# Performance work log

Hardware: AMD Instinct MI355X
Metric: run time of the kernel (lower is better)

## Reference

```python
import jax, jax.numpy as jnp
import numpy as np

# Irreps structure (hardcoded per init_kwargs):
#  input  = 16x0e + 8x1o  -> dim 16 + 8*3 = 40
#  query  = key = 8x0e + 4x1o -> dim 8 + 4*3 = 20
#  output = 16x0e + 8x1o -> dim 40
#  edge_sh = 1x0e + 1x1o -> dim 4
M0, M1 = 16, 8          # input multiplicities (scalar, vector)
Q0, Q1 = 8, 4           # query/key multiplicities
O0, O1 = 16, 8          # output multiplicities
TPK_NUMEL = M0*Q0 + M1*Q0 + M0*Q1 + M1*Q1 + M1*Q1   # 320
TPV_NUMEL = M0*O0 + M1*O0 + M0*O1 + M1*O1 + M1*O1   # 640
EDGE_BASIS = 16
HIDDEN = 32


def _split(x):
    """Split irreps vector [*, m0 + 3*m1] into scalars [*, m0] and vectors [*, m1, 3]."""
    m0 = x.shape[-1] - 3 * ((x.shape[-1] - M0) // 3) if False else None
    return x  # placeholder, not used


def fc_net(x, w1, w2):
    """e3nn FullyConnectedNet: no biases, 1/sqrt(fan_in) scaling, silu hidden act."""
    h = jax.nn.silu((x @ w1) * (1.0 / np.sqrt(x.shape[-1])))
    return (h @ w2) * (1.0 / np.sqrt(w1.shape[-1]))


def fctp_edge(xs, xv, shs, shv, w, o0, o1):
    """FullyConnectedTensorProduct((m0x0e+m1x1o) x (1x0e+1x1o) -> (o0x0e+o1x1o))
    with per-edge weights w [E, numel]. Component-normalized CG, path-normalized output.
    xs:[E,m0] xv:[E,m1,3] shs:[E,1] shv:[E,3]."""
    m0, m1 = xs.shape[1], xv.shape[1]
    sizes = [m0*o0, m1*o0, m0*o1, m1*o1, m1*o1]
    offs = np.cumsum([0] + sizes)
    w1 = w[:, offs[0]:offs[1]].reshape(-1, m0, o0)
    w2 = w[:, offs[1]:offs[2]].reshape(-1, m1, o0)
    w3 = w[:, offs[2]:offs[3]].reshape(-1, m0, o1)
    w4 = w[:, offs[3]:offs[4]].reshape(-1, m1, o1)
    w5 = w[:, offs[4]:offs[5]].reshape(-1, m1, o1)
    # scalar output paths: 0e x 0e -> 0e ; 1o x 1o -> 0e (dot / sqrt3)
    p_ss = xs * shs                                            # [E,m0]
    p_vv = jnp.einsum('eic,ec->ei', xv, shv) * (1.0/np.sqrt(3.0))  # [E,m1]
    out_s = (jnp.einsum('ei,eio->eo', p_ss, w1)
             + jnp.einsum('ei,eio->eo', p_vv, w2)) * (1.0/np.sqrt(m0 + m1))
    # vector output paths: 0e x 1o ; 1o x 0e ; 1o x 1o -> 1o (cross / sqrt2)
    p_sv = xs[:, :, None] * shv[:, None, :]                    # [E,m0,3]
    p_vs = xv * shs[:, :, None]                                # [E,m1,3]
    p_xx = jnp.cross(xv, shv[:, None, :]) * (1.0/np.sqrt(2.0)) # [E,m1,3]
    out_v = (jnp.einsum('eic,eio->eoc', p_sv, w3)
             + jnp.einsum('eic,eio->eoc', p_vs, w4)
             + jnp.einsum('eic,eio->eoc', p_xx, w5)) * (1.0/np.sqrt(m0 + 2*m1))
    return out_s, out_v


def setup_inputs() -> dict:
    key = jax.random.key(0)
    ks = jax.random.split(key, 12)
    N, E = 10000, 100000
    node_ft = jax.random.normal(ks[0], (N, M0 + 3*M1), dtype=jnp.float32)
    edge_index = jax.random.randint(ks[1], (2, E), 0, N, dtype=jnp.int64)
    edge_sh = jax.random.normal(ks[2], (E, 4), dtype=jnp.float32)
    edge_scalars = jax.random.uniform(ks[3], (E, EDGE_BASIS), dtype=jnp.float32)
    # learned parameters
    w_q_s = jax.random.normal(ks[4], (M0, Q0), dtype=jnp.float32)
    w_q_v = jax.random.normal(ks[5], (M1, Q1), dtype=jnp.float32)
    fck_w1 = jax.random.normal(ks[6], (EDGE_BASIS, HIDDEN), dtype=jnp.float32)
    fck_w2 = jax.random.normal(ks[7], (HIDDEN, TPK_NUMEL), dtype=jnp.float32)
    fcv_w1 = jax.random.normal(ks[8], (EDGE_BASIS, HIDDEN), dtype=jnp.float32)
    fcv_w2 = jax.random.normal(ks[9], (HIDDEN, TPV_NUMEL), dtype=jnp.float32)
    wdot_s = jax.random.normal(ks[10], (Q0, Q0), dtype=jnp.float32)
    wdot_v = jax.random.normal(ks[11], (Q1, Q1), dtype=jnp.float32)
    return dict(node_ft=node_ft, edge_index=edge_index, edge_sh=edge_sh,
                edge_scalars=edge_scalars, w_q_s=w_q_s, w_q_v=w_q_v,
                fck_w1=fck_w1, fck_w2=fck_w2, fcv_w1=fcv_w1, fcv_w2=fcv_w2,
                wdot_s=wdot_s, wdot_v=wdot_v)


def reference(node_ft, edge_index, edge_sh, edge_scalars, w_q_s, w_q_v,
              fck_w1, fck_w2, fcv_w1, fcv_w2, wdot_s, wdot_v):
    N = node_ft.shape[0]
    sender, receiver = edge_index[0], edge_index[1]
    x_s = node_ft[:, :M0]                       # [N,16]
    x_v = node_ft[:, M0:].reshape(N, M1, 3)     # [N,8,3]
    # q = o3.Linear(input -> query): per-irrep linear mixing, 1/sqrt(mul) norm
    q_s = (x_s @ w_q_s) * (1.0/np.sqrt(M0))                    # [N,Q0]
    q_v = jnp.einsum('nic,io->noc', x_v, w_q_v) * (1.0/np.sqrt(M1))  # [N,Q1,3]
    sh_s, sh_v = edge_sh[:, :1], edge_sh[:, 1:4]
    xs_e, xv_e = x_s[sender], x_v[sender]       # gather sender features
    # per-edge tensor-product weights from radial MLPs
    wk = fc_net(edge_scalars, fck_w1, fck_w2)   # [E, 320]
    wv = fc_net(edge_scalars, fcv_w1, fcv_w2)   # [E, 640]
    k_s, k_v = fctp_edge(xs_e, xv_e, sh_s, sh_v, wk, Q0, Q1)
    v_s, v_v = fctp_edge(xs_e, xv_e, sh_s, sh_v, wv, O0, O1)
    # dot = FCTP(query, key -> 0e) with shared internal weights
    qr_s, qr_v = q_s[receiver], q_v[receiver]
    fan = Q0*Q0 + Q1*Q1
    dot = (jnp.einsum('ei,ej,ij->e', qr_s, k_s, wdot_s)
           + jnp.einsum('eic,ejc,ij->e', qr_v, k_v, wdot_v) * (1.0/np.sqrt(3.0))
           ) * (1.0/np.sqrt(fan))               # [E]
    # scatter-softmax over receiver
    ex = jnp.exp(dot)
    z = jax.ops.segment_sum(ex, receiver, num_segments=N)      # [N]
    alpha = ex / z[receiver]
    a = jnp.sqrt(jax.nn.relu(alpha))            # [E]
    out_s = jax.ops.segment_sum(a[:, None] * v_s, receiver, num_segments=N)
    out_v = jax.ops.segment_sum(a[:, None, None] * v_v, receiver, num_segments=N)
    return jnp.concatenate([out_s, out_v.reshape(N, O1*3)], axis=-1)  # [N,40]
```

## Files before the change

kernel.cpp:

```cpp
#include <hip/hip_runtime.h>


#define BS 256
#define EPB 64

typedef _Float16 h2 __attribute__((ext_vector_type(2)));

__device__ __forceinline__ float silu_f(float x) {
    return x * (1.0f / (1.0f + __expf(-x)));
}
__device__ __forceinline__ unsigned short f2h(float f) {
    return __builtin_bit_cast(unsigned short, (_Float16)f);
}
__device__ __forceinline__ unsigned pk2h(float a, float b) {
    return (unsigned)f2h(a) | ((unsigned)f2h(b) << 16);
}
__device__ __forceinline__ h2 uh2(unsigned u) {
    return __builtin_bit_cast(h2, u);
}
__device__ __forceinline__ h2 pkrtz(float a, float b) {
    return __builtin_bit_cast(h2, __builtin_amdgcn_cvt_pkrtz(a, b));
}
__device__ __forceinline__ h2 pfma(h2 a, h2 b, h2 c) {
    return __builtin_elementwise_fma(a, b, c);
}
__device__ __forceinline__ float h2s(h2 a) {
    return (float)a[0] + (float)a[1];
}
__device__ __forceinline__ float wred4(float v) {
    v += __shfl_xor(v, 16);
    v += __shfl_xor(v, 32);
    return v;
}

__global__ __launch_bounds__(256) void pre_count(
    const float* __restrict__ node_ft,
    const int*   __restrict__ ei,
    const float* __restrict__ w_q_s, const float* __restrict__ w_q_v,
    const float* __restrict__ wdot_s, const float* __restrict__ wdot_v,
    const float* __restrict__ fck_w2, const float* __restrict__ fcv_w2,
    float* __restrict__ qd, int* __restrict__ cnt, int* __restrict__ flag,
    uint4* __restrict__ pk,
    int N, int E)
{
    const int gid = blockIdx.x * blockDim.x + threadIdx.x;

    int acc = 0;
    if ((threadIdx.x & 63) == 0) {
        const int kmax = (E < 64) ? E : 64;
        for (int k = 0; k < kmax; ++k) acc |= ei[2*k + 1];
    }
    acc = __shfl(acc, 0, 64);
    const int is64 = (acc == 0) ? 1 : 0;
    if (gid == 0) *flag = is64;

    if (gid < E) {
        const int rcv = is64 ? ei[2*(E + gid)] : ei[E + gid];
        atomicAdd(cnt + rcv, 1);
    }

    if (gid < 3840) {
        uint4 r;
        if (gid < 1280) {
            const int pg = gid / 320;
            const int local = gid - pg * 320;
            if (local < 128) {
                const int j = local >> 2, rr = local & 3, ip = rr >> 1, h = rr & 1;
                const int i0 = 4*pg + 2*ip;
                const float* s0 = fck_w2 + j*320 + i0*8 + 4*h;
                const float* s1 = s0 + 8;
                r = make_uint4(pk2h(s0[0], s1[0]), pk2h(s0[1], s1[1]),
                               pk2h(s0[2], s1[2]), pk2h(s0[3], s1[3]));
            } else if (local < 192) {
                const int l = local - 128; const int j = l >> 1, ip = l & 1;
                const int i0 = 4*pg + 2*ip;
                const float* s0 = fck_w2 + j*320 + 192 + i0*4;
                const float* s1 = s0 + 4;
                r = make_uint4(pk2h(s0[0], s1[0]), pk2h(s0[1], s1[1]),
                               pk2h(s0[2], s1[2]), pk2h(s0[3], s1[3]));
            } else if (local < 256) {
                const int l = local - 192; const int j = l >> 1, h = l & 1;
                const int i0 = 2*pg;
                const float* s0 = fck_w2 + j*320 + 128 + i0*8 + 4*h;
                const float* s1 = s0 + 8;
                r = make_uint4(pk2h(s0[0], s1[0]), pk2h(s0[1], s1[1]),
                               pk2h(s0[2], s1[2]), pk2h(s0[3], s1[3]));
            } else {
                const int l = local - 256; const int jp = l >> 2, rr = l & 3;
                const int il = rr >> 1, h = rr & 1;
                const int i = 2*pg + il, j0 = 2*jp;
                const int col = (h == 0 ? 256 : 288) + i*4;
                const float* s0 = fck_w2 + j0*320 + col;
                const float* s1 = s0 + 320;
                r = make_uint4(pk2h(s0[0], s1[0]), pk2h(s0[1], s1[1]),
                               pk2h(s0[2], s1[2]), pk2h(s0[3], s1[3]));
            }
        } else if (gid < 2816) {
            const int l2 = gid - 1280;
            const int pg = l2 / 384;
            const int local = l2 - pg * 384;
            const float* s0;
            const float* s1;
            if (local < 256) {
                const int j = local >> 3, rr = local & 7, ip = rr >> 2, h = rr & 3;
                const int i0 = 4*pg + 2*ip;
                s0 = fcv_w2 + j*640 + i0*16 + h*4;
                s1 = s0 + 16;
            } else {
                const int l = local - 256; const int j = l >> 2, h = l & 3;
                const int i0 = 2*pg;
                s0 = fcv_w2 + j*640 + 256 + i0*16 + h*4;
                s1 = s0 + 16;
            }
            r = make_uint4(pk2h(s0[0], s1[0]), pk2h(s0[1], s1[1]),
                           pk2h(s0[2], s1[2]), pk2h(s0[3], s1[3]));
        } else {
            const int l2 = gid - 2816;
            const int pg = l2 >> 8;
            const int local = l2 & 255;
            const float* s0;
            const float* s1;
            if (local < 128) {
                const int j = local >> 2, rr = local & 3, ip = rr >> 1, h = rr & 1;
                const int i0 = 4*pg + 2*ip;
                s0 = fcv_w2 + j*640 + 384 + i0*8 + 4*h;
                s1 = s0 + 8;
            } else {
                const int l = local - 128;
                const int jp = l >> 3, rr = l & 7, il = rr >> 2, h2c = rr & 3;
                const int i = 2*pg + il, j0 = 2*jp;
                const int base = (h2c < 2) ? 512 : 576;
                s0 = fcv_w2 + j0*640 + base + i*8 + (h2c & 1)*4;
                s1 = s0 + 640;
            }
            r = make_uint4(pk2h(s0[0], s1[0]), pk2h(s0[1], s1[1]),
                           pk2h(s0[2], s1[2]), pk2h(s0[3], s1[3]));
        }
        pk[gid] = r;
    }

    const int n = gid;
    if (n >= N) return;

    const float* nf = node_ft + (size_t)n * 40;
    float xs[16];
#pragma unroll
    for (int i = 0; i < 16; ++i) xs[i] = nf[i];
    float qv0[8];
#pragma unroll
    for (int o = 0; o < 8; ++o) {
        float a = 0.f;
#pragma unroll
        for (int i = 0; i < 16; ++i) a += xs[i] * w_q_s[i*8 + o];
        qv0[o] = a * 0.25f;
    }
    float* qdn = qd + (size_t)n * 20;
#pragma unroll
    for (int j = 0; j < 8; ++j) {
        float a = 0.f;
#pragma unroll
        for (int i = 0; i < 8; ++i) a += qv0[i] * wdot_s[i*8 + j];
        qdn[j] = a;
    }
    float xv[8][3];
#pragma unroll
    for (int i = 0; i < 8; ++i)
#pragma unroll
        for (int c = 0; c < 3; ++c) xv[i][c] = nf[16 + i*3 + c];
    float qv[4][3];
#pragma unroll
    for (int o = 0; o < 4; ++o)
#pragma unroll
        for (int c = 0; c < 3; ++c) {
            float a = 0.f;
#pragma unroll
            for (int i = 0; i < 8; ++i) a += xv[i][c] * w_q_v[i*4 + o];
            qv[o][c] = a * 0.35355339059327379f;
        }
#pragma unroll
    for (int j = 0; j < 4; ++j)
#pragma unroll
        for (int c = 0; c < 3; ++c) {
            float a = 0.f;
#pragma unroll
            for (int i = 0; i < 4; ++i) a += qv[i][c] * wdot_v[i*4 + j];
            qdn[8 + j*3 + c] = a;
        }
}

__global__ __launch_bounds__(1024) void scan_kernel(
    const int* __restrict__ cnt, int* __restrict__ start,
    int* __restrict__ cursor, int N)
{
    __shared__ int wsum[16];
    __shared__ int s_carry;
    const int tid = threadIdx.x, wave = tid >> 6, lane = tid & 63;
    if (tid == 0) s_carry = 0;
    __syncthreads();
    for (int base = 0; base < N; base += 1024) {
        const int i = base + tid;
        const int v = (i < N) ? cnt[i] : 0;
        int x = v;
#pragma unroll
        for (int d = 1; d < 64; d <<= 1) {
            const int y = __shfl_up(x, d, 64);
            if (lane >= d) x += y;
        }
        if (lane == 63) wsum[wave] = x;
        __syncthreads();
        if (wave == 0 && lane < 16) {
            int w = wsum[lane];
#pragma unroll
            for (int d = 1; d < 16; d <<= 1) {
                const int y = __shfl_up(w, d, 64);
                if (lane >= d) w += y;
            }
            wsum[lane] = w;
        }
        __syncthreads();
        const int woff = (wave == 0) ? 0 : wsum[wave - 1];
        const int carry = s_carry;
        if (i < N) {
            const int s = carry + woff + x - v;
            start[i] = s;
            cursor[i] = s;
        }
        __syncthreads();
        if (tid == 0) s_carry = carry + wsum[15];
        __syncthreads();
    }
    if (tid == 0) start[N] = s_carry;
}

__global__ __launch_bounds__(BS) void edge_all(
    const float* __restrict__ node_ft,
    const int*   __restrict__ ei,
    const float* __restrict__ edge_sh,
    const float* __restrict__ edge_scalars,
    const float* __restrict__ fck_w1,
    const float* __restrict__ fcv_w1,
    const uint4* __restrict__ pk,
    const float* __restrict__ qd,
    int*   __restrict__ cursor,
    float* __restrict__ vbuf,
    const int* __restrict__ flag,
    int N, int E)
{
    __shared__ uint4 swz[4 * 385];

    const int tid = threadIdx.x;
    const int lane = tid & 63;
    const int p = lane >> 4;
    const int q = lane & 15;
    const int w = tid >> 6;
    const int e = blockIdx.x * EPB + w * 16 + q;
    const bool val = (e < E);
    const int ec = val ? e : (E - 1);

    const int is64 = *flag;
    const int snd = is64 ? ei[2*ec]       : ei[ec];
    const int rcv = is64 ? ei[2*(E + ec)] : ei[E + ec];

    int pos = 0;
    if (p == 0 && val) pos = atomicAdd(cursor + rcv, 1);

    const float4 s4 = *(const float4*)(edge_sh + (size_t)ec * 4);
    const float sh_s = s4.x;
    const float sh_v[3] = {s4.y, s4.z, s4.w};
    const float* nf = node_ft + (size_t)snd * 40;
    const float c3 = 0.57735026918962576f;
    const float c7 = 0.70710678118654752f;

    float es[16];
    {
        const float4* a0 = (const float4*)(edge_scalars + (size_t)ec * 16);
#pragma unroll
        for (int t = 0; t < 4; ++t) {
            const float4 v = a0[t];
            es[4*t+0]=v.x; es[4*t+1]=v.y; es[4*t+2]=v.z; es[4*t+3]=v.w;
        }
    }

#pragma unroll
    for (int it = 0; it < 5; ++it) {
        const int idx = it * BS + tid;
        const int pg = idx / 320;
        swz[pg * 321 + (idx - pg * 320)] = pk[idx];
    }

    float sa = 0.f;
    float hk[32];
#pragma unroll
    for (int j = 0; j < 32; ++j) {
        float a = 0.f;
#pragma unroll
        for (int t = 0; t < 16; ++t) a += es[t] * fck_w1[t*32 + j];
        hk[j] = silu_f(a * 0.25f);
    }
    __syncthreads();

    {
        const uint4* g = swz + p * 321;

        const h2 xs01 = pkrtz(nf[4*p + 0], nf[4*p + 1]);
        const h2 xs23 = pkrtz(nf[4*p + 2], nf[4*p + 3]);
        const float x00 = nf[16 + 6*p], x01 = nf[17 + 6*p], x02 = nf[18 + 6*p];
        const float x10 = nf[19 + 6*p], x11 = nf[20 + 6*p], x12 = nf[21 + 6*p];
        const h2 pvp = pkrtz((x00*sh_v[0] + x01*sh_v[1] + x02*sh_v[2]) * c3,
                             (x10*sh_v[0] + x11*sh_v[1] + x12*sh_v[2]) * c3);

        h2 K1[8] = {}, K3[4] = {}, K2[8] = {};
#pragma unroll
        for (int j = 0; j < 32; ++j) {
            const uint4 A = g[j*4+0], B = g[j*4+1], C = g[j*4+2], D = g[j*4+3];
            const uint4 Ea = g[128 + j*2], Fb = g[128 + j*2 + 1];
            const uint4 U = g[192 + j*2], V = g[192 + j*2 + 1];
            const h2 hh = pkrtz(hk[j], hk[j]);
            const h2 t01 = hh * xs01, t23 = hh * xs23, tp = hh * pvp;
            K1[0]=pfma(t01,uh2(A.x),K1[0]); K1[0]=pfma(t23,uh2(C.x),K1[0]);
            K1[1]=pfma(t01,uh2(A.y),K1[1]); K1[1]=pfma(t23,uh2(C.y),K1[1]);
            K1[2]=pfma(t01,uh2(A.z),K1[2]); K1[2]=pfma(t23,uh2(C.z),K1[2]);
            K1[3]=pfma(t01,uh2(A.w),K1[3]); K1[3]=pfma(t23,uh2(C.w),K1[3]);
            K1[4]=pfma(t01,uh2(B.x),K1[4]); K1[4]=pfma(t23,uh2(D.x),K1[4]);
            K1[5]=pfma(t01,uh2(B.y),K1[5]); K1[5]=pfma(t23,uh2(D.y),K1[5]);
            K1[6]=pfma(t01,uh2(B.z),K1[6]); K1[6]=pfma(t23,uh2(D.z),K1[6]);
            K1[7]=pfma(t01,uh2(B.w),K1[7]); K1[7]=pfma(t23,uh2(D.w),K1[7]);
            K3[0]=pfma(t01,uh2(Ea.x),K3[0]); K3[0]=pfma(t23,uh2(Fb.x),K3[0]);
            K3[1]=pfma(t01,uh2(Ea.y),K3[1]); K3[1]=pfma(t23,uh2(Fb.y),K3[1]);
            K3[2]=pfma(t01,uh2(Ea.z),K3[2]); K3[2]=pfma(t23,uh2(Fb.z),K3[2]);
            K3[3]=pfma(t01,uh2(Ea.w),K3[3]); K3[3]=pfma(t23,uh2(Fb.w),K3[3]);
            K2[0]=pfma(tp,uh2(U.x),K2[0]); K2[1]=pfma(tp,uh2(U.y),K2[1]);
            K2[2]=pfma(tp,uh2(U.z),K2[2]); K2[3]=pfma(tp,uh2(U.w),K2[3]);
            K2[4]=pfma(tp,uh2(V.x),K2[4]); K2[5]=pfma(tp,uh2(V.y),K2[5]);
            K2[6]=pfma(tp,uh2(V.z),K2[6]); K2[7]=pfma(tp,uh2(V.w),K2[7]);
        }

        h2 P4[8] = {}, P5[8] = {};
#pragma unroll
        for (int jp = 0; jp < 16; ++jp) {
            const uint4 a4 = g[256 + jp*4 + 0];
            const uint4 b4 = g[256 + jp*4 + 1];
            const uint4 c4 = g[256 + jp*4 + 2];
            const uint4 d4 = g[256 + jp*4 + 3];
            const h2 hp = pkrtz(hk[2*jp], hk[2*jp+1]);
            P4[0]=pfma(hp,uh2(a4.x),P4[0]); P4[1]=pfma(hp,uh2(a4.y),P4[1]);
            P4[2]=pfma(hp,uh2(a4.z),P4[2]); P4[3]=pfma(hp,uh2(a4.w),P4[3]);
            P5[0]=pfma(hp,uh2(b4.x),P5[0]); P5[1]=pfma(hp,uh2(b4.y),P5[1]);
            P5[2]=pfma(hp,uh2(b4.z),P5[2]); P5[3]=pfma(hp,uh2(b4.w),P5[3]);
            P4[4]=pfma(hp,uh2(c4.x),P4[4]); P4[5]=pfma(hp,uh2(c4.y),P4[5]);
            P4[6]=pfma(hp,uh2(c4.z),P4[6]); P4[7]=pfma(hp,uh2(c4.w),P4[7]);
            P5[4]=pfma(hp,uh2(d4.x),P5[4]); P5[5]=pfma(hp,uh2(d4.y),P5[5]);
            P5[6]=pfma(hp,uh2(d4.z),P5[6]); P5[7]=pfma(hp,uh2(d4.w),P5[7]);
        }

        float ds = 0.f, dv = 0.f;
        {
            float qdr[20];
            const float4* rp = (const float4*)(qd + (size_t)rcv * 20);
#pragma unroll
            for (int t = 0; t < 5; ++t) {
                const float4 a = rp[t];
                qdr[4*t+0]=a.x; qdr[4*t+1]=a.y; qdr[4*t+2]=a.z; qdr[4*t+3]=a.w;
            }
#pragma unroll
            for (int o = 0; o < 8; ++o)
                ds += qdr[o] * (sh_s*h2s(K1[o]) + h2s(K2[o]));
            float KV[12] = {};
            {
                const float s0=sh_s*x00, s1=sh_s*x01, s2=sh_s*x02;
                const float cx0=c7*(x01*sh_v[2]-x02*sh_v[1]);
                const float cx1=c7*(x02*sh_v[0]-x00*sh_v[2]);
                const float cx2=c7*(x00*sh_v[1]-x01*sh_v[0]);
#pragma unroll
                for (int o = 0; o < 4; ++o) {
                    const float w4 = h2s(P4[o]), w5 = h2s(P5[o]);
                    KV[o*3+0] += s0*w4 + cx0*w5;
                    KV[o*3+1] += s1*w4 + cx1*w5;
                    KV[o*3+2] += s2*w4 + cx2*w5;
                }
            }
            {
                const float s0=sh_s*x10, s1=sh_s*x11, s2=sh_s*x12;
                const float cx0=c7*(x11*sh_v[2]-x12*sh_v[1]);
                const float cx1=c7*(x12*sh_v[0]-x10*sh_v[2]);
                const float cx2=c7*(x10*sh_v[1]-x11*sh_v[0]);
#pragma unroll
                for (int o = 0; o < 4; ++o) {
                    const float w4 = h2s(P4[4+o]), w5 = h2s(P5[4+o]);
                    KV[o*3+0] += s0*w4 + cx0*w5;
                    KV[o*3+1] += s1*w4 + cx1*w5;
                    KV[o*3+2] += s2*w4 + cx2*w5;
                }
            }
#pragma unroll
            for (int o = 0; o < 4; ++o) {
                const float k3 = h2s(K3[o]);
#pragma unroll
                for (int c = 0; c < 3; ++c)
                    dv += qdr[8 + o*3 + c] * (k3*sh_v[c] + KV[o*3+c]);
            }
        }
        ds = wred4(ds); dv = wred4(dv);

        if (p == 0 && val) {
            const float dot = ds * 4.0343567508008e-3f + dv * 2.0171788261497e-3f;
            sa = __expf(0.5f * dot);
            vbuf[(size_t)pos * 44 + 40] = sa * sa;
        }
    }

    __syncthreads();
#pragma unroll
    for (int it = 0; it < 6; ++it) {
        const int idx = it * BS + tid;
        const int pg = idx / 384;
        swz[pg * 385 + (idx - pg * 384)] = pk[1280 + idx];
    }

    float hv[32];
#pragma unroll
    for (int j = 0; j < 32; ++j) {
        float a = 0.f;
#pragma unroll
        for (int t = 0; t < 16; ++t) a += es[t] * fcv_w1[t*32 + j];
        hv[j] = silu_f(a * 0.25f);
    }
    __syncthreads();

    {
        const uint4* g = swz + p * 385;

        const h2 xs01 = pkrtz(nf[4*p + 0]*sh_s, nf[4*p + 1]*sh_s);
        const h2 xs23 = pkrtz(nf[4*p + 2]*sh_s, nf[4*p + 3]*sh_s);
        const h2 pvp = pkrtz(
            (nf[16+6*p]*sh_v[0] + nf[17+6*p]*sh_v[1] + nf[18+6*p]*sh_v[2]) * c3,
            (nf[19+6*p]*sh_v[0] + nf[20+6*p]*sh_v[1] + nf[21+6*p]*sh_v[2]) * c3);

        h2 Aa[16] = {};
#pragma unroll
        for (int j = 0; j < 32; ++j) {
            const uint4* gw = g + j*8;
            const uint4 a0 = gw[0], a1 = gw[1], a2 = gw[2], a3 = gw[3];
            const uint4 b0 = gw[4], b1 = gw[5], b2 = gw[6], b3 = gw[7];
            const uint4* g2 = g + 256 + j*4;
            const uint4 u0 = g2[0], u1 = g2[1], u2 = g2[2], u3 = g2[3];
            const h2 hh = pkrtz(hv[j], hv[j]);
            const h2 t01 = hh * xs01, t23 = hh * xs23, tp = hh * pvp;
            Aa[0] =pfma(t01,uh2(a0.x),Aa[0]);  Aa[0] =pfma(t23,uh2(b0.x),Aa[0]);  Aa[0] =pfma(tp,uh2(u0.x),Aa[0]);
            Aa[1] =pfma(t01,uh2(a0.y),Aa[1]);  Aa[1] =pfma(t23,uh2(b0.y),Aa[1]);  Aa[1] =pfma(tp,uh2(u0.y),Aa[1]);
            Aa[2] =pfma(t01,uh2(a0.z),Aa[2]);  Aa[2] =pfma(t23,uh2(b0.z),Aa[2]);  Aa[2] =pfma(tp,uh2(u0.z),Aa[2]);
            Aa[3] =pfma(t01,uh2(a0.w),Aa[3]);  Aa[3] =pfma(t23,uh2(b0.w),Aa[3]);  Aa[3] =pfma(tp,uh2(u0.w),Aa[3]);
            Aa[4] =pfma(t01,uh2(a1.x),Aa[4]);  Aa[4] =pfma(t23,uh2(b1.x),Aa[4]);  Aa[4] =pfma(tp,uh2(u1.x),Aa[4]);
            Aa[5] =pfma(t01,uh2(a1.y),Aa[5]);  Aa[5] =pfma(t23,uh2(b1.y),Aa[5]);  Aa[5] =pfma(tp,uh2(u1.y),Aa[5]);
            Aa[6] =pfma(t01,uh2(a1.z),Aa[6]);  Aa[6] =pfma(t23,uh2(b1.z),Aa[6]);  Aa[6] =pfma(tp,uh2(u1.z),Aa[6]);
            Aa[7] =pfma(t01,uh2(a1.w),Aa[7]);  Aa[7] =pfma(t23,uh2(b1.w),Aa[7]);  Aa[7] =pfma(tp,uh2(u1.w),Aa[7]);
            Aa[8] =pfma(t01,uh2(a2.x),Aa[8]);  Aa[8] =pfma(t23,uh2(b2.x),Aa[8]);  Aa[8] =pfma(tp,uh2(u2.x),Aa[8]);
            Aa[9] =pfma(t01,uh2(a2.y),Aa[9]);  Aa[9] =pfma(t23,uh2(b2.y),Aa[9]);  Aa[9] =pfma(tp,uh2(u2.y),Aa[9]);
            Aa[10]=pfma(t01,uh2(a2.z),Aa[10]); Aa[10]=pfma(t23,uh2(b2.z),Aa[10]); Aa[10]=pfma(tp,uh2(u2.z),Aa[10]);
            Aa[11]=pfma(t01,uh2(a2.w),Aa[11]); Aa[11]=pfma(t23,uh2(b2.w),Aa[11]); Aa[11]=pfma(tp,uh2(u2.w),Aa[11]);
            Aa[12]=pfma(t01,uh2(a3.x),Aa[12]); Aa[12]=pfma(t23,uh2(b3.x),Aa[12]); Aa[12]=pfma(tp,uh2(u3.x),Aa[12]);
            Aa[13]=pfma(t01,uh2(a3.y),Aa[13]); Aa[13]=pfma(t23,uh2(b3.y),Aa[13]); Aa[13]=pfma(tp,uh2(u3.y),Aa[13]);
            Aa[14]=pfma(t01,uh2(a3.z),Aa[14]); Aa[14]=pfma(t23,uh2(b3.z),Aa[14]); Aa[14]=pfma(tp,uh2(u3.z),Aa[14]);
            Aa[15]=pfma(t01,uh2(a3.w),Aa[15]); Aa[15]=pfma(t23,uh2(b3.w),Aa[15]); Aa[15]=pfma(tp,uh2(u3.w),Aa[15]);
        }

        float A0[16];
#pragma unroll
        for (int o = 0; o < 16; ++o) A0[o] = wred4(h2s(Aa[o]));

        if (p == 0 && val) {
            const float cs = 0.03608439182435161f;
            float4* vp = (float4*)(vbuf + (size_t)pos * 44);
#pragma unroll
            for (int t = 0; t < 4; ++t) {
                float4 r;
                r.x = sa * A0[4*t+0] * cs; r.y = sa * A0[4*t+1] * cs;
                r.z = sa * A0[4*t+2] * cs; r.w = sa * A0[4*t+3] * cs;
                vp[t] = r;
            }
        }
    }

    __syncthreads();
#pragma unroll
    for (int it = 0; it < 4; ++it) {
        const int idx = it * BS + tid;
        const int pg = idx >> 8;
        swz[pg * 257 + (idx & 255)] = pk[2816 + idx];
    }
    __syncthreads();

    {
        const uint4* g = swz + p * 257;

        const h2 xs01 = pkrtz(nf[4*p + 0], nf[4*p + 1]);
        const h2 xs23 = pkrtz(nf[4*p + 2], nf[4*p + 3]);

        h2 T3[8] = {};
#pragma unroll
        for (int j = 0; j < 32; ++j) {
            const uint4 E0 = g[j*4+0], E1 = g[j*4+1];
            const uint4 F0 = g[j*4+2], F1 = g[j*4+3];
            const h2 hh = pkrtz(hv[j], hv[j]);
            const h2 t01 = hh * xs01, t23 = hh * xs23;
            T3[0]=pfma(t01,uh2(E0.x),T3[0]); T3[0]=pfma(t23,uh2(F0.x),T3[0]);
            T3[1]=pfma(t01,uh2(E0.y),T3[1]); T3[1]=pfma(t23,uh2(F0.y),T3[1]);
            T3[2]=pfma(t01,uh2(E0.z),T3[2]); T3[2]=pfma(t23,uh2(F0.z),T3[2]);
            T3[3]=pfma(t01,uh2(E0.w),T3[3]); T3[3]=pfma(t23,uh2(F0.w),T3[3]);
            T3[4]=pfma(t01,uh2(E1.x),T3[4]); T3[4]=pfma(t23,uh2(F1.x),T3[4]);
            T3[5]=pfma(t01,uh2(E1.y),T3[5]); T3[5]=pfma(t23,uh2(F1.y),T3[5]);
            T3[6]=pfma(t01,uh2(E1.z),T3[6]); T3[6]=pfma(t23,uh2(F1.z),T3[6]);
            T3[7]=pfma(t01,uh2(E1.w),T3[7]); T3[7]=pfma(t23,uh2(F1.w),T3[7]);
        }

        h2 P4[16] = {}, P5[16] = {};
#pragma unroll
        for (int jp = 0; jp < 16; ++jp) {
            const uint4* gw = g + 128 + jp*8;
            const uint4 a4 = gw[0], b4 = gw[1];
            const uint4 c4 = gw[2], d4 = gw[3];
            const uint4 e4 = gw[4], f4 = gw[5];
            const uint4 m4 = gw[6], n4 = gw[7];
            const h2 hp = pkrtz(hv[2*jp], hv[2*jp+1]);
            P4[0] =pfma(hp,uh2(a4.x),P4[0]);  P4[1] =pfma(hp,uh2(a4.y),P4[1]);
            P4[2] =pfma(hp,uh2(a4.z),P4[2]);  P4[3] =pfma(hp,uh2(a4.w),P4[3]);
            P4[4] =pfma(hp,uh2(b4.x),P4[4]);  P4[5] =pfma(hp,uh2(b4.y),P4[5]);
            P4[6] =pfma(hp,uh2(b4.z),P4[6]);  P4[7] =pfma(hp,uh2(b4.w),P4[7]);
            P5[0] =pfma(hp,uh2(c4.x),P5[0]);  P5[1] =pfma(hp,uh2(c4.y),P5[1]);
            P5[2] =pfma(hp,uh2(c4.z),P5[2]);  P5[3] =pfma(hp,uh2(c4.w),P5[3]);
            P5[4] =pfma(hp,uh2(d4.x),P5[4]);  P5[5] =pfma(hp,uh2(d4.y),P5[5]);
            P5[6] =pfma(hp,uh2(d4.z),P5[6]);  P5[7] =pfma(hp,uh2(d4.w),P5[7]);
            P4[8] =pfma(hp,uh2(e4.x),P4[8]);  P4[9] =pfma(hp,uh2(e4.y),P4[9]);
            P4[10]=pfma(hp,uh2(e4.z),P4[10]); P4[11]=pfma(hp,uh2(e4.w),P4[11]);
            P4[12]=pfma(hp,uh2(f4.x),P4[12]); P4[13]=pfma(hp,uh2(f4.y),P4[13]);
            P4[14]=pfma(hp,uh2(f4.z),P4[14]); P4[15]=pfma(hp,uh2(f4.w),P4[15]);
            P5[8] =pfma(hp,uh2(m4.x),P5[8]);  P5[9] =pfma(hp,uh2(m4.y),P5[9]);
            P5[10]=pfma(hp,uh2(m4.z),P5[10]); P5[11]=pfma(hp,uh2(m4.w),P5[11]);
            P5[12]=pfma(hp,uh2(n4.x),P5[12]); P5[13]=pfma(hp,uh2(n4.y),P5[13]);
            P5[14]=pfma(hp,uh2(n4.z),P5[14]); P5[15]=pfma(hp,uh2(n4.w),P5[15]);
        }

        float R[24], T3f[8];
        {
            float acc[24];
#pragma unroll
            for (int o = 0; o < 24; ++o) acc[o] = 0.f;
            {
                const float x0 = nf[16 + 6*p], x1 = nf[17 + 6*p], x2 = nf[18 + 6*p];
                const float s0 = sh_s*x0, s1 = sh_s*x1, s2 = sh_s*x2;
                const float cx0 = c7*(x1*sh_v[2] - x2*sh_v[1]);
                const float cx1 = c7*(x2*sh_v[0] - x0*sh_v[2]);
                const float cx2 = c7*(x0*sh_v[1] - x1*sh_v[0]);
#pragma unroll
                for (int o = 0; o < 8; ++o) {
                    const float w4 = h2s(P4[o]), w5 = h2s(P5[o]);
                    acc[o*3+0] += s0*w4 + cx0*w5;
                    acc[o*3+1] += s1*w4 + cx1*w5;
                    acc[o*3+2] += s2*w4 + cx2*w5;
                }
            }
            {
                const float x0 = nf[19 + 6*p], x1 = nf[20 + 6*p], x2 = nf[21 + 6*p];
                const float s0 = sh_s*x0, s1 = sh_s*x1, s2 = sh_s*x2;
                const float cx0 = c7*(x1*sh_v[2] - x2*sh_v[1]);
                const float cx1 = c7*(x2*sh_v[0] - x0*sh_v[2]);
                const float cx2 = c7*(x0*sh_v[1] - x1*sh_v[0]);
#pragma unroll
                for (int o = 0; o < 8; ++o) {
                    const float w4 = h2s(P4[8+o]), w5 = h2s(P5[8+o]);
                    acc[o*3+0] += s0*w4 + cx0*w5;
                    acc[o*3+1] += s1*w4 + cx1*w5;
                    acc[o*3+2] += s2*w4 + cx2*w5;
                }
            }
#pragma unroll
            for (int o = 0; o < 24; ++o) R[o] = wred4(acc[o]);
        }
#pragma unroll
        for (int o = 0; o < 8; ++o) T3f[o] = wred4(h2s(T3[o]));

        if (p == 0 && val) {
            const float sc = 0.03125f;
            float row[24];
#pragma unroll
            for (int o = 0; o < 8; ++o)
#pragma unroll
                for (int c = 0; c < 3; ++c)
                    row[o*3+c] = sa * (T3f[o]*sh_v[c] + R[o*3+c]) * sc;
            float4* vp = (float4*)(vbuf + (size_t)pos * 44 + 16);
#pragma unroll
            for (int t = 0; t < 6; ++t) {
                float4 r; r.x = row[4*t+0]; r.y = row[4*t+1]; r.z = row[4*t+2]; r.w = row[4*t+3];
                vp[t] = r;
            }
        }
    }
}

__global__ __launch_bounds__(256) void node_reduce(
    const int*   __restrict__ start,
    const float* __restrict__ vbuf,
    float* __restrict__ out, int N)
{
    const int wave = threadIdx.x >> 6;
    const int lane = threadIdx.x & 63;
    const int n = blockIdx.x * 4 + wave;
    if (n >= N) return;
    const int r0 = start[n], r1 = start[n + 1];
    float z = 0.f, comp = 0.f;
    for (int r = r0; r < r1; ++r) {
        const float* row = vbuf + (size_t)r * 44;
        z += row[40];
        if (lane < 40) comp += row[lane];
    }
    if (lane < 40)
        out[(size_t)n * 40 + lane] = (z > 0.f) ? comp * rsqrtf(z) : 0.f;
}

extern "C" void kernel_launch(void* const* d_in, const int* in_sizes, int n_in,
                              void* d_out, int out_size, void* d_ws, size_t ws_size,
                              hipStream_t stream) {
    const float* node_ft      = (const float*)d_in[0];
    const int*   edge_index   = (const int*)  d_in[1];
    const float* edge_sh      = (const float*)d_in[2];
    const float* edge_scalars = (const float*)d_in[3];
    const float* w_q_s        = (const float*)d_in[4];
    const float* w_q_v        = (const float*)d_in[5];
    const float* fck_w1       = (const float*)d_in[6];
    const float* fck_w2       = (const float*)d_in[7];
    const float* fcv_w1       = (const float*)d_in[8];
    const float* fcv_w2       = (const float*)d_in[9];
    const float* wdot_s       = (const float*)d_in[10];
    const float* wdot_v       = (const float*)d_in[11];

    const int N = in_sizes[0] / 40;
    const int E = in_sizes[2] / 4;

    float* ws    = (float*)d_ws;
    float* qd    = ws;
    int*   cnt   = (int*)(ws + (size_t)N * 20);
    int*   start = cnt + N;
    int*   curs  = start + N + 1;
    int*   flg   = curs + N;
    size_t off   = (size_t)N * 20 + N + (N + 1) + N + 1;
    off = (off + 3) & ~(size_t)3;
    uint4* pk    = (uint4*)(ws + off);
    float* vbuf  = ws + off + 15360;

    float* out = (float*)d_out;

    const int NE = (E > N) ? E : N;
    const int EB = (E + EPB - 1) / EPB;

    hipMemsetAsync(cnt, 0, (size_t)N * sizeof(int), stream);
    hipLaunchKernelGGL(pre_count, dim3((NE + 255) / 256), dim3(256), 0, stream,
                       node_ft, edge_index, w_q_s, w_q_v, wdot_s, wdot_v,
                       fck_w2, fcv_w2, qd, cnt, flg, pk, N, E);
    hipLaunchKernelGGL(scan_kernel, dim3(1), dim3(1024), 0, stream,
                       cnt, start, curs, N);
    hipLaunchKernelGGL(edge_all, dim3(EB), dim3(BS), 0, stream,
                       node_ft, edge_index, edge_sh, edge_scalars,
                       fck_w1, fcv_w1, pk, qd, curs, vbuf, flg, N, E);
    hipLaunchKernelGGL(node_reduce, dim3((N + 3) / 4), dim3(256), 0, stream,
                       start, vbuf, out, N);
}
```

Baseline: 240.8 us.

## Replace counting-sort CSR reduction with direct float atomic accumulation per receiver

Removes the receiver count atomics, the single-block prefix scan kernel, the cursor slot assignment and the per-row edge buffer. Each edge now atomically adds its 40 output components and its softmax denominator straight into a per-node accumulator, and a final normalize kernel scales by rsqrt of the denominator. This saves one launch, a serial scan, and the write and reread of the edge buffer. In exchange it issues 41 float atomics per edge, which can contend on high-degree nodes and makes the summation order nondeterministic.

Measured after the change: 339.6 us. 1.41x slower.

```diff
diff --git a/kernel.cpp b/kernel.cpp
--- a/kernel.cpp
+++ b/kernel.cpp
@@ -39,24 +39,17 @@
     const float* __restrict__ w_q_s, const float* __restrict__ w_q_v,
     const float* __restrict__ wdot_s, const float* __restrict__ wdot_v,
     const float* __restrict__ fck_w2, const float* __restrict__ fcv_w2,
-    float* __restrict__ qd, int* __restrict__ cnt, int* __restrict__ flag,
+    float* __restrict__ qd, int* __restrict__ flag,
     uint4* __restrict__ pk,
     int N, int E)
 {
     const int gid = blockIdx.x * blockDim.x + threadIdx.x;
 
-    int acc = 0;
-    if ((threadIdx.x & 63) == 0) {
+    if (gid == 0) {
+        int acc = 0;
         const int kmax = (E < 64) ? E : 64;
         for (int k = 0; k < kmax; ++k) acc |= ei[2*k + 1];
-    }
-    acc = __shfl(acc, 0, 64);
-    const int is64 = (acc == 0) ? 1 : 0;
-    if (gid == 0) *flag = is64;
-
-    if (gid < E) {
-        const int rcv = is64 ? ei[2*(E + gid)] : ei[E + gid];
-        atomicAdd(cnt + rcv, 1);
+        *flag = (acc == 0) ? 1 : 0;
     }
 
     if (gid < 3840) {
@@ -188,50 +181,6 @@
         }
 }
 
-__global__ __launch_bounds__(1024) void scan_kernel(
-    const int* __restrict__ cnt, int* __restrict__ start,
-    int* __restrict__ cursor, int N)
-{
-    __shared__ int wsum[16];
-    __shared__ int s_carry;
-    const int tid = threadIdx.x, wave = tid >> 6, lane = tid & 63;
-    if (tid == 0) s_carry = 0;
-    __syncthreads();
-    for (int base = 0; base < N; base += 1024) {
-        const int i = base + tid;
-        const int v = (i < N) ? cnt[i] : 0;
-        int x = v;
-#pragma unroll
-        for (int d = 1; d < 64; d <<= 1) {
-            const int y = __shfl_up(x, d, 64);
-            if (lane >= d) x += y;
-        }
-        if (lane == 63) wsum[wave] = x;
-        __syncthreads();
-        if (wave == 0 && lane < 16) {
-            int w = wsum[lane];
-#pragma unroll
-            for (int d = 1; d < 16; d <<= 1) {
-                const int y = __shfl_up(w, d, 64);
-                if (lane >= d) w += y;
-            }
-            wsum[lane] = w;
-        }
-        __syncthreads();
-        const int woff = (wave == 0) ? 0 : wsum[wave - 1];
-        const int carry = s_carry;
-        if (i < N) {
-            const int s = carry + woff + x - v;
-            start[i] = s;
-            cursor[i] = s;
-        }
-        __syncthreads();
-        if (tid == 0) s_carry = carry + wsum[15];
-        __syncthreads();
-    }
-    if (tid == 0) start[N] = s_carry;
-}
-
 __global__ __launch_bounds__(BS) void edge_all(
     const float* __restrict__ node_ft,
     const int*   __restrict__ ei,
@@ -241,8 +190,7 @@
     const float* __restrict__ fcv_w1,
     const uint4* __restrict__ pk,
     const float* __restrict__ qd,
-    int*   __restrict__ cursor,
-    float* __restrict__ vbuf,
+    float* __restrict__ acc,
     const int* __restrict__ flag,
     int N, int E)
 {
@@ -261,15 +209,13 @@
     const int snd = is64 ? ei[2*ec]       : ei[ec];
     const int rcv = is64 ? ei[2*(E + ec)] : ei[E + ec];
 
-    int pos = 0;
-    if (p == 0 && val) pos = atomicAdd(cursor + rcv, 1);
-
     const float4 s4 = *(const float4*)(edge_sh + (size_t)ec * 4);
     const float sh_s = s4.x;
     const float sh_v[3] = {s4.y, s4.z, s4.w};
     const float* nf = node_ft + (size_t)snd * 40;
     const float c3 = 0.57735026918962576f;
     const float c7 = 0.70710678118654752f;
+    float* ap = acc + (size_t)rcv * 44;
 
     float es[16];
     {
@@ -405,7 +351,7 @@
         if (p == 0 && val) {
             const float dot = ds * 4.0343567508008e-3f + dv * 2.0171788261497e-3f;
             sa = __expf(0.5f * dot);
-            vbuf[(size_t)pos * 44 + 40] = sa * sa;
+            atomicAdd(ap + 40, sa * sa);
         }
     }
 
@@ -470,14 +416,9 @@
 
         if (p == 0 && val) {
             const float cs = 0.03608439182435161f;
-            float4* vp = (float4*)(vbuf + (size_t)pos * 44);
-#pragma unroll
-            for (int t = 0; t < 4; ++t) {
-                float4 r;
-                r.x = sa * A0[4*t+0] * cs; r.y = sa * A0[4*t+1] * cs;
-                r.z = sa * A0[4*t+2] * cs; r.w = sa * A0[4*t+3] * cs;
-                vp[t] = r;
-            }
+#pragma unroll
+            for (int o = 0; o < 16; ++o)
+                atomicAdd(ap + o, sa * A0[o] * cs);
         }
     }
 
@@ -542,9 +483,9 @@
 
         float R[24], T3f[8];
         {
-            float acc[24];
-#pragma unroll
-            for (int o = 0; o < 24; ++o) acc[o] = 0.f;
+            float acc2[24];
+#pragma unroll
+            for (int o = 0; o < 24; ++o) acc2[o] = 0.f;
             {
                 const float x0 = nf[16 + 6*p], x1 = nf[17 + 6*p], x2 = nf[18 + 6*p];
                 const float s0 = sh_s*x0, s1 = sh_s*x1, s2 = sh_s*x2;
@@ -554,9 +495,9 @@
 #pragma unroll
                 for (int o = 0; o < 8; ++o) {
                     const float w4 = h2s(P4[o]), w5 = h2s(P5[o]);
-                    acc[o*3+0] += s0*w4 + cx0*w5;
-                    acc[o*3+1] += s1*w4 + cx1*w5;
-                    acc[o*3+2] += s2*w4 + cx2*w5;
+                    acc2[o*3+0] += s0*w4 + cx0*w5;
+                    acc2[o*3+1] += s1*w4 + cx1*w5;
+                    acc2[o*3+2] += s2*w4 + cx2*w5;
                 }
             }
             {
@@ -568,53 +509,41 @@
 #pragma unroll
                 for (int o = 0; o < 8; ++o) {
                     const float w4 = h2s(P4[8+o]), w5 = h2s(P5[8+o]);
-                    acc[o*3+0] += s0*w4 + cx0*w5;
-                    acc[o*3+1] += s1*w4 + cx1*w5;
-                    acc[o*3+2] += s2*w4 + cx2*w5;
+                    acc2[o*3+0] += s0*w4 + cx0*w5;
+                    acc2[o*3+1] += s1*w4 + cx1*w5;
+                    acc2[o*3+2] += s2*w4 + cx2*w5;
                 }
             }
 #pragma unroll
-            for (int o = 0; o < 24; ++o) R[o] = wred4(acc[o]);
+            for (int o = 0; o < 24; ++o) R[o] = wred4(acc2[o]);
         }
 #pragma unroll
         for (int o = 0; o < 8; ++o) T3f[o] = wred4(h2s(T3[o]));
 
         if (p == 0 && val) {
             const float sc = 0.03125f;
-            float row[24];
 #pragma unroll
             for (int o = 0; o < 8; ++o)
 #pragma unroll
                 for (int c = 0; c < 3; ++c)
-                    row[o*3+c] = sa * (T3f[o]*sh_v[c] + R[o*3+c]) * sc;
-            float4* vp = (float4*)(vbuf + (size_t)pos * 44 + 16);
-#pragma unroll
-            for (int t = 0; t < 6; ++t) {
-                float4 r; r.x = row[4*t+0]; r.y = row[4*t+1]; r.z = row[4*t+2]; r.w = row[4*t+3];
-                vp[t] = r;
-            }
-        }
-    }
-}
-
-__global__ __launch_bounds__(256) void node_reduce(
-    const int*   __restrict__ start,
-    const float* __restrict__ vbuf,
+                    atomicAdd(ap + 16 + o*3 + c,
+                              sa * (T3f[o]*sh_v[c] + R[o*3+c]) * sc);
+        }
+    }
+}
+
+__global__ __launch_bounds__(256) void normalize(
+    const float* __restrict__ acc,
     float* __restrict__ out, int N)
 {
     const int wave = threadIdx.x >> 6;
     const int lane = threadIdx.x & 63;
     const int n = blockIdx.x * 4 + wave;
     if (n >= N) return;
-    const int r0 = start[n], r1 = start[n + 1];
-    float z = 0.f, comp = 0.f;
-    for (int r = r0; r < r1; ++r) {
-        const float* row = vbuf + (size_t)r * 44;
-        z += row[40];
-        if (lane < 40) comp += row[lane];
-    }
+    const float z = acc[(size_t)n * 44 + 40];
     if (lane < 40)
-        out[(size_t)n * 40 + lane] = (z > 0.f) ? comp * rsqrtf(z) : 0.f;
+        out[(size_t)n * 40 + lane] =
+            (z > 0.f) ? acc[(size_t)n * 44 + lane] * rsqrtf(z) : 0.f;
 }
 
 extern "C" void kernel_launch(void* const* d_in, const int* in_sizes, int n_in,
@@ -638,29 +567,24 @@
 
     float* ws    = (float*)d_ws;
     float* qd    = ws;
-    int*   cnt   = (int*)(ws + (size_t)N * 20);
-    int*   start = cnt + N;
-    int*   curs  = start + N + 1;
-    int*   flg   = curs + N;
-    size_t off   = (size_t)N * 20 + N + (N + 1) + N + 1;
+    int*   flg   = (int*)(ws + (size_t)N * 20);
+    size_t off   = (size_t)N * 20 + 1;
     off = (off + 3) & ~(size_t)3;
     uint4* pk    = (uint4*)(ws + off);
-    float* vbuf  = ws + off + 15360;
+    float* acc   = ws + off + 15360;
 
     float* out = (float*)d_out;
 
-    const int NE = (E > N) ? E : N;
+    const int NE = (N > 3840) ? N : 3840;
     const int EB = (E + EPB - 1) / EPB;
 
-    hipMemsetAsync(cnt, 0, (size_t)N * sizeof(int), stream);
+    hipMemsetAsync(acc, 0, (size_t)N * 44 * sizeof(float), stream);
     hipLaunchKernelGGL(pre_count, dim3((NE + 255) / 256), dim3(256), 0, stream,
                        node_ft, edge_index, w_q_s, w_q_v, wdot_s, wdot_v,
-                       fck_w2, fcv_w2, qd, cnt, flg, pk, N, E);
-    hipLaunchKernelGGL(scan_kernel, dim3(1), dim3(1024), 0, stream,
-                       cnt, start, curs, N);
+                       fck_w2, fcv_w2, qd, flg, pk, N, E);
     hipLaunchKernelGGL(edge_all, dim3(EB), dim3(BS), 0, stream,
                        node_ft, edge_index, edge_sh, edge_scalars,
-                       fck_w1, fcv_w1, pk, qd, curs, vbuf, flg, N, E);
-    hipLaunchKernelGGL(node_reduce, dim3((N + 3) / 4), dim3(256), 0, stream,
-                       start, vbuf, out, N);
-}
+                       fck_w1, fcv_w1, pk, qd, acc, flg, N, E);
+    hipLaunchKernelGGL(normalize, dim3((N + 3) / 4), dim3(256), 0, stream,
+                       acc, out, N);
+}
```
